# Optimization experiments

Measured on AMD Instinct MI355X. Metric: run time of the kernel, lower is better.

## Reference

```python
import jax, jax.numpy as jnp
import numpy as np

B, NAV, H, W = 16, 36, 120, 160
HID, AEMB, NF = 512, 32, 4

def _conv(x, w, b, stride, pad, dil, groups):
    y = jax.lax.conv_general_dilated(x, w, stride, pad, rhs_dilation=dil, feature_group_count=groups)
    return y + b[None, :, None, None]

def _avgpool(x, k, s):
    y = jax.lax.reduce_window(x, 0.0, jax.lax.add, (1, 1) + k, (1, 1) + s, 'VALID')
    return y / float(k[0] * k[1])

def _conv2_block(x, w1, b1, w2, b2):
    # conv2_1: k5 stride (5,7) dilation 10 -> avgpool 3/3 -> conv2_2: k3 stride 2 dilation (1,2) -> avgpool (3,9)/3
    y = _conv(x, w1, b1, (5, 7), ((0, 0), (0, 0)), (10, 10), 1)
    y = _avgpool(y, (3, 3), (3, 3))
    y = _conv(y, w2, b2, (2, 2), ((0, 0), (0, 0)), (1, 2), 1)
    y = _avgpool(y, (3, 9), (3, 3))
    return y[:, 0]  # [B,3,12]

def setup_inputs() -> dict:
    key = jax.random.key(0)
    ks = jax.random.split(key, 24)
    s = 0.02
    d = {}
    d['depth_feat_0'] = jax.random.normal(ks[0], (B, NAV, H, W), jnp.float32)
    d['depth_feat_1'] = jax.random.normal(ks[1], (B, NAV, H, W), jnp.float32)
    d['obj_detection_feat'] = jax.random.normal(ks[2], (B, NAV, H, W), jnp.float32)
    d['num_navigable_feat'] = jax.random.uniform(ks[3], (B, NAV), jnp.float32)
    d['pre_action_feat'] = jax.random.normal(ks[4], (B, AEMB), jnp.float32)
    d['h_0'] = jax.random.normal(ks[5], (B, HID), jnp.float32)
    d['c_0'] = jax.random.normal(ks[6], (B, HID), jnp.float32)
    d['weighted_ctx'] = jax.random.normal(ks[7], (B, HID), jnp.float32)
    d['navigable_index'] = jax.random.randint(ks[8], (B, 8), 0, NAV).astype(jnp.int32)
    # params
    d['conv1_w'] = jax.random.normal(ks[9], (NAV, 2, 5, 5), jnp.float32) * s
    d['conv1_b'] = jnp.zeros((NAV,), jnp.float32)
    d['dyn_filters'] = jax.random.normal(ks[10], (NF, NAV, 2, 5, 5), jnp.float32) * s
    d['dyn_w1'] = jax.random.normal(ks[11], (HID, HID // 4), jnp.float32) * s
    d['dyn_b1'] = jnp.zeros((HID // 4,), jnp.float32)
    d['dyn_w2'] = jax.random.normal(ks[12], (HID // 4, NF), jnp.float32) * s
    d['dyn_b2'] = jnp.zeros((NF,), jnp.float32)
    d['conv2_1_w'] = jax.random.normal(ks[13], (1, 1, 5, 5), jnp.float32) * s
    d['conv2_1_b'] = jnp.zeros((1,), jnp.float32)
    d['conv2_2_w'] = jax.random.normal(ks[14], (1, 1, 3, 3), jnp.float32) * s
    d['conv2_2_b'] = jnp.zeros((1,), jnp.float32)
    in_sz = HID + NAV + NF + AEMB  # 584
    d['lstm_w_ih'] = jax.random.normal(ks[15], (4 * HID, in_sz), jnp.float32) * s
    d['lstm_w_hh'] = jax.random.normal(ks[16], (4 * HID, HID), jnp.float32) * s
    d['lstm_b_ih'] = jnp.zeros((4 * HID,), jnp.float32)
    d['lstm_b_hh'] = jnp.zeros((4 * HID,), jnp.float32)
    return d

def reference(depth_feat_0, depth_feat_1, obj_detection_feat, num_navigable_feat, pre_action_feat, h_0, c_0, weighted_ctx, navigable_index, conv1_w, conv1_b, dyn_filters, dyn_w1, dyn_b1, dyn_w2, dyn_b2, conv2_1_w, conv2_1_b, conv2_2_w, conv2_2_b, lstm_w_ih, lstm_w_hh, lstm_b_ih, lstm_b_hh):
    Bv = depth_feat_0.shape[0]
    # interleave depth channels: [B,72,H,W] (replaces 36-iter python copy loop)
    mid1 = jnp.stack([depth_feat_0, depth_feat_1], axis=2).reshape(Bv, 2 * NAV, H, W)
    total_depth = _conv(mid1, conv1_w, conv1_b, (1, 1), ((2, 2), (2, 2)), (1, 1), NAV)  # [B,36,H,W]
    nav_attn = jax.nn.softmax(num_navigable_feat, axis=1)[:, :, None, None]
    mid2 = jnp.stack([total_depth * nav_attn, obj_detection_feat * nav_attn], axis=2).reshape(Bv, 2 * NAV, H, W)
    # dynamic conv: per-sample filter = attention-weighted mix of NF learned grouped filters
    filt_attn = jax.nn.softmax(jax.nn.relu(weighted_ctx @ dyn_w1 + dyn_b1) @ dyn_w2 + dyn_b2, axis=1)  # [B,4]
    kern = jnp.einsum('bf,fgikl->bgikl', filt_attn, dyn_filters).reshape(Bv * NAV, 2, 5, 5)
    dyn_out = jax.lax.conv_general_dilated(mid2.reshape(1, Bv * 2 * NAV, H, W), kern, (1, 1), ((2, 2), (2, 2)), feature_group_count=Bv * NAV).reshape(Bv, NAV, H, W)
    # panorama canvas assembly: tile i -> row block (2 - i//12), col i%12
    canvas = dyn_out.reshape(Bv, 3, 12, H, W)[:, ::-1].transpose(0, 1, 3, 2, 4).reshape(Bv, 1, 3 * H, 12 * W)
    v1 = _conv2_block(canvas, conv2_1_w, conv2_1_b, conv2_2_w, conv2_2_b)
    rolled = jnp.concatenate([canvas[..., -W:], canvas[..., :-W]], axis=-1)
    v2 = _conv2_block(rolled, conv2_1_w, conv2_1_b, conv2_2_w, conv2_2_b)
    v2 = jnp.concatenate([v2[:, :, 1:], v2[:, :, :1]], axis=-1)
    vf = ((v1 + v2) * 0.5)[:, ::-1].reshape(Bv, NAV)  # flip row dim then flatten
    vf = jax.nn.softmax(vf / 10.0, axis=1)  # self.softmax_temperature hardcoded to 10
    concat = jnp.concatenate([weighted_ctx, vf, filt_attn, pre_action_feat], axis=1)
    gates = concat @ lstm_w_ih.T + lstm_b_ih + h_0 @ lstm_w_hh.T + lstm_b_hh
    i, f, g, o = jnp.split(gates, 4, axis=1)
    c_1 = jax.nn.sigmoid(f) * c_0 + jax.nn.sigmoid(i) * jnp.tanh(g)
    h_1 = jax.nn.sigmoid(o) * jnp.tanh(c_1)
    mask = jnp.zeros((Bv, NAV + 1), jnp.float32).at[:, 0].set(1.0)
    mask = mask.at[jnp.arange(Bv)[:, None], navigable_index + 1].set(1.0)
    return (h_1, c_1, vf, mask)
```

## Files before the change

### kernel.cpp

```cpp
#include <hip/hip_runtime.h>
#include <math.h>

#define B_ 16
#define NAV_ 36
#define H_ 120
#define W_ 160
#define HID_ 512
#define PLANES (B_*NAV_)
#define PLANE_PX (H_*W_)
#define CANVAS_H 360
#define CANVAS_W 1920
#define CANVAS_PX (CANVAS_H*CANVAS_W)

#define OUT_H 12
#define IN_ROWS 20
#define TD_ROWS 16
#define OBJ_ROWS 16
#define ROWB 352
#define INCH (IN_ROWS*ROWB)

#define WS_NAV    0
#define WS_FATT   576
#define WS_KERN   640
#define WS_TD     29440
#define WS_CANVAS (WS_TD + PLANES*PLANE_PX)
#define WS_POOL1  (WS_CANVAS + B_*CANVAS_PX)
#define WS_VF     (WS_POOL1 + B_*2*19*89)

typedef unsigned int u32;
typedef _Float16 h2_t __attribute__((ext_vector_type(2)));
typedef float float4a __attribute__((ext_vector_type(4), aligned(4)));

__device__ __forceinline__ float sigmoidf_(float x) { return 1.f / (1.f + expf(-x)); }

__device__ __forceinline__ u32 pkh(float a, float b) {
    return __builtin_bit_cast(u32, __builtin_amdgcn_cvt_pkrtz(a, b));
}
__device__ __forceinline__ float dot2h(u32 a, u32 b, float c) {
#if __has_builtin(__builtin_amdgcn_fdot2)
    return __builtin_amdgcn_fdot2(__builtin_bit_cast(h2_t, a),
                                  __builtin_bit_cast(h2_t, b), c, false);
#else
    float r;
    asm("v_dot2_f32_f16 %0, %1, %2, %3" : "=v"(r) : "v"(a), "v"(b), "v"(c));
    return r;
#endif
}

__device__ __forceinline__ void conv8(const unsigned char* b0, const unsigned char* b1,
                                      const u32* ew, float* acc)
{
    #pragma unroll
    for (int ky = 0; ky < 5; ++ky) {
        const int off = ky*ROWB;
        int4 qa = *(const int4*)(b0 + off);
        int2 qb = *(const int2*)(b0 + off + 16);
        int4 ra = *(const int4*)(b1 + off);
        int2 rb = *(const int2*)(b1 + off + 16);
        u32 P[6] = {(u32)qa.x,(u32)qa.y,(u32)qa.z,(u32)qa.w,(u32)qb.x,(u32)qb.y};
        u32 Q[6] = {(u32)ra.x,(u32)ra.y,(u32)ra.z,(u32)ra.w,(u32)rb.x,(u32)rb.y};
        const u32 e0 = ew[ky*3+0], e1 = ew[ky*3+1], e2 = ew[ky*3+2];
        const u32 f0 = ew[15+ky*3+0], f1 = ew[15+ky*3+1], f2 = ew[15+ky*3+2];
        const u32 o0 = e0 << 16;
        const u32 o1 = __builtin_amdgcn_alignbit(e1, e0, 16);
        const u32 o2 = __builtin_amdgcn_alignbit(e2, e1, 16);
        const u32 g0 = f0 << 16;
        const u32 g1 = __builtin_amdgcn_alignbit(f1, f0, 16);
        const u32 g2 = __builtin_amdgcn_alignbit(f2, f1, 16);
        #pragma unroll
        for (int m = 0; m < 4; ++m) {
            acc[2*m]   = dot2h(e0, P[m], dot2h(e1, P[m+1], dot2h(e2, P[m+2], acc[2*m])));
            acc[2*m+1] = dot2h(o0, P[m], dot2h(o1, P[m+1], dot2h(o2, P[m+2], acc[2*m+1])));
            acc[2*m]   = dot2h(f0, Q[m], dot2h(f1, Q[m+1], dot2h(f2, Q[m+2], acc[2*m])));
            acc[2*m+1] = dot2h(g0, Q[m], dot2h(g1, Q[m+1], dot2h(g2, Q[m+2], acc[2*m+1])));
        }
    }
}

#define LOAD_EW(EW, SW)                                                        \
    {                                                                          \
        _Pragma("unroll")                                                      \
        for (int q = 0; q < 7; ++q) {                                          \
            int4 t_ = ((const int4*)(SW))[q];                                  \
            EW[4*q]=(u32)t_.x; EW[4*q+1]=(u32)t_.y; EW[4*q+2]=(u32)t_.z; EW[4*q+3]=(u32)t_.w; \
        }                                                                      \
        int2 t_ = ((const int2*)(SW))[14];                                     \
        EW[28]=(u32)t_.x; EW[29]=(u32)t_.y;                                    \
    }

__global__ __launch_bounds__(256)
void k_pre(const float* __restrict__ wctx, const float* __restrict__ dw1,
           const float* __restrict__ db1, const float* __restrict__ dw2,
           const float* __restrict__ db2, const float* __restrict__ dynf,
           const float* __restrict__ numnav, float* __restrict__ ws)
{
    const int tid = threadIdx.x;
    const int b = blockIdx.x;
    __shared__ float sh[128];
    __shared__ float sred[8];
    __shared__ float nv[36];
    __shared__ float nms[2];
    if (tid < 128) {
        float acc = db1[tid];
        for (int k = 0; k < HID_; ++k) acc += wctx[b*HID_ + k] * dw1[k*128 + tid];
        sh[tid] = fmaxf(acc, 0.f);
    }
    __syncthreads();
    if (tid < 4) {
        float acc = db2[tid];
        for (int j = 0; j < 128; ++j) acc += sh[j] * dw2[j*4 + tid];
        sred[tid] = acc;
    }
    __syncthreads();
    if (tid == 0) {
        float m = fmaxf(fmaxf(sred[0], sred[1]), fmaxf(sred[2], sred[3]));
        float e0 = expf(sred[0]-m), e1 = expf(sred[1]-m), e2 = expf(sred[2]-m), e3 = expf(sred[3]-m);
        float s = e0+e1+e2+e3;
        sred[4] = e0/s; sred[5] = e1/s; sred[6] = e2/s; sred[7] = e3/s;
        ws[WS_FATT + b*4+0] = sred[4]; ws[WS_FATT + b*4+1] = sred[5];
        ws[WS_FATT + b*4+2] = sred[6]; ws[WS_FATT + b*4+3] = sred[7];
    }
    __syncthreads();
    {
        const float fa0 = sred[4], fa1 = sred[5], fa2 = sred[6], fa3 = sred[7];
        for (int e = tid; e < 1800; e += 256) {
            float v = fa0*dynf[e] + fa1*dynf[1800+e] + fa2*dynf[3600+e] + fa3*dynf[5400+e];
            ws[WS_KERN + b*1800 + e] = v;
        }
    }
    if (tid < 36) nv[tid] = numnav[b*NAV_ + tid];
    __syncthreads();
    if (tid == 0) {
        float m = nv[0];
        for (int i = 1; i < 36; ++i) m = fmaxf(m, nv[i]);
        float s = 0.f;
        for (int i = 0; i < 36; ++i) s += expf(nv[i]-m);
        nms[0] = m; nms[1] = s;
    }
    __syncthreads();
    if (tid < 36) ws[WS_NAV + b*NAV_ + tid] = expf(nv[tid]-nms[0]) / nms[1];
}

__global__ __launch_bounds__(256)
void k_fused(const float* __restrict__ d0, const float* __restrict__ d1,
             const float* __restrict__ obj, const float* __restrict__ conv1_w,
             const float* __restrict__ conv1_b, float* __restrict__ ws)
{
    const int tid = threadIdx.x;
    const int band = blockIdx.x;
    const int plane = blockIdx.y;
    const int b = plane / NAV_;
    const int g = plane % NAV_;
    const int r0 = band * OUT_H;

    __shared__ __align__(16) unsigned char smem[2*INCH + OBJ_ROWS*ROWB + TD_ROWS*ROWB + 256];
    unsigned char* inL  = smem;
    unsigned char* objL = smem + 2*INCH;
    unsigned char* tdL  = objL + OBJ_ROWS*ROWB;
    u32* wts = (u32*)(tdL + TD_ROWS*ROWB);

    if (tid < 30) {
        const int ch = tid/15, ky = (tid%15)/3, k = tid%3;
        const float* wsrc = conv1_w + g*50 + ch*25 + ky*5;
        wts[tid] = pkh(wsrc[2*k], (k < 2) ? wsrc[2*k+1] : 0.f);
    } else if (tid >= 32 && tid < 62) {
        const int t2 = tid - 32;
        const int ch = t2/15, ky = (t2%15)/3, k = t2%3;
        const float* wsrc = ws + WS_KERN + plane*50 + ch*25 + ky*5;
        wts[tid] = pkh(wsrc[2*k], (k < 2) ? wsrc[2*k+1] : 0.f);
    } else if (tid == 62) ((float*)wts)[62] = conv1_b[g];
    else if (tid == 63)   ((float*)wts)[63] = ws[WS_NAV + plane];

    const float* pd0 = d0 + (size_t)plane*PLANE_PX;
    const float* pd1 = d1 + (size_t)plane*PLANE_PX;
    const float* pob = obj + (size_t)plane*PLANE_PX;
    for (int i = tid; i < 2*IN_ROWS*44 + OBJ_ROWS*44; i += 256) {
        const float* src; unsigned char* dst; int row, j, gr;
        if (i < 2*IN_ROWS*44) {
            const int ch = i/(IN_ROWS*44), rem = i%(IN_ROWS*44);
            row = rem/44; j = rem%44; gr = r0 - 4 + row;
            src = ch ? pd1 : pd0;
            dst = inL + (size_t)ch*INCH + row*ROWB + j*8;
        } else {
            const int k = i - 2*IN_ROWS*44;
            row = k/44; j = k%44; gr = r0 - 2 + row;
            src = pob;
            dst = objL + row*ROWB + j*8;
        }
        u32 lo = 0, hi = 0;
        if ((unsigned)gr < (unsigned)H_ && j <= 40) {
            const float* sp = src + gr*W_;
            if (j == 0) hi = pkh(sp[0], sp[1]);
            else if (j < 40) { const float4a v = *(const float4a*)(sp + 4*j - 2);
                               lo = pkh(v.x, v.y);  hi = pkh(v.z, v.w); }
            else lo = pkh(sp[158], sp[159]);
        }
        *(int2*)dst = make_int2((int)lo, (int)hi);
    }
    if (tid < 32) {
        const int rr = tid >> 1;
        *(u32*)(tdL + rr*ROWB + ((tid & 1) ? 324 : 0)) = 0;
    }
    __syncthreads();

    for (int t = tid; t < TD_ROWS*20; t += 256) {
        const int tr = t/20, s = t%20;
        const int gr = r0 - 2 + tr;
        u32* rowp = (u32*)(tdL + tr*ROWB);
        if ((unsigned)gr >= (unsigned)H_) {
            rowp[4*s+1] = 0;
            *(int2*)(rowp + 4*s + 2) = make_int2(0, 0);
            rowp[4*s+4] = 0;
            continue;
        }
        float acc[8];
        #pragma unroll
        for (int p = 0; p < 8; ++p) acc[p] = 0.f;
        u32 ew[30];
        LOAD_EW(ew, wts)
        conv8(inL + tr*ROWB + s*16, inL + INCH + tr*ROWB + s*16, ew, acc);
        const float bias = ((const float*)wts)[62];
        const u32 p0 = pkh(acc[0]+bias, acc[1]+bias);
        const u32 p1 = pkh(acc[2]+bias, acc[3]+bias);
        const u32 p2 = pkh(acc[4]+bias, acc[5]+bias);
        const u32 p3 = pkh(acc[6]+bias, acc[7]+bias);
        rowp[4*s+1] = p0;
        *(int2*)(rowp + 4*s + 2) = make_int2((int)p1, (int)p2);
        rowp[4*s+4] = p3;
    }
    __syncthreads();

    if (tid < OUT_H*20) {
        const int yr = tid/20, s = tid%20;
        float acc[8];
        #pragma unroll
        for (int p = 0; p < 8; ++p) acc[p] = 0.f;
        u32 ew[30];
        LOAD_EW(ew, wts + 32)
        conv8(tdL + yr*ROWB + s*16, objL + yr*ROWB + s*16, ew, acc);
        const float a = ((const float*)wts)[63];
        const int rowblk = 2 - g/12;
        const int colblk = g % 12;
        float* cbase = ws + WS_CANVAS + (size_t)b*CANVAS_PX
                     + (size_t)(rowblk*H_ + r0 + yr)*CANVAS_W + colblk*W_ + s*8;
        *(float4*)cbase     = make_float4(a*acc[0], a*acc[1], a*acc[2], a*acc[3]);
        *(float4*)(cbase+4) = make_float4(a*acc[4], a*acc[5], a*acc[6], a*acc[7]);
    }
}

__global__ __launch_bounds__(256)
void k_conv2a(const float* __restrict__ w21p, const float* __restrict__ b21p,
              float* __restrict__ ws)
{
    const int blk = blockIdx.x;
    const int a = blk % 19;
    const int bv = blk / 19;
    const int ver = bv & 1;
    const int b = bv >> 1;
    const int coloff = ver ? (CANVAS_W - W_) : 0;

    __shared__ float s1[3*267];
    __shared__ float swt[25];
    if (threadIdx.x < 25) swt[threadIdx.x] = w21p[threadIdx.x];
    __syncthreads();
    const float b21 = b21p[0];
    const float* cv = ws + WS_CANVAS + (size_t)b*CANVAS_PX;

    for (int px = threadIdx.x; px < 3*267; px += 256) {
        const int row = px / 267;
        const int v = px % 267;
        const int u = 3*a + row;
        float acc = b21;
        #pragma unroll
        for (int ky = 0; ky < 5; ++ky) {
            const float* rp = cv + (5*u + 10*ky)*CANVAS_W;
            #pragma unroll
            for (int kx = 0; kx < 5; ++kx) {
                int c = 7*v + 10*kx + coloff;
                if (c >= CANVAS_W) c -= CANVAS_W;
                acc += swt[ky*5+kx] * rp[c];
            }
        }
        s1[px] = acc;
    }
    __syncthreads();
    if (threadIdx.x < 89) {
        const int bb = threadIdx.x;
        float s = 0.f;
        #pragma unroll
        for (int i = 0; i < 3; ++i)
            #pragma unroll
            for (int j = 0; j < 3; ++j)
                s += s1[i*267 + 3*bb + j];
        ws[WS_POOL1 + blk*89 + bb] = s * (1.f/9.f);
    }
}

__global__ __launch_bounds__(256)
void k_conv2b(const float* __restrict__ w22p, const float* __restrict__ b22p,
              const int* __restrict__ navidx, float* __restrict__ ws,
              float* __restrict__ out)
{
    const int b = blockIdx.x;
    __shared__ float p[2*19*89];
    __shared__ float s2[2*9*43];
    __shared__ float svf[36];
    __shared__ float sms[2];
    __shared__ float swt[9];

    for (int i = threadIdx.x; i < 2*19*89; i += 256)
        p[i] = ws[WS_POOL1 + (b*2)*19*89 + i];
    if (threadIdx.x < 9) swt[threadIdx.x] = w22p[threadIdx.x];
    const float b22 = b22p[0];
    __syncthreads();

    for (int t = threadIdx.x; t < 2*9*43; t += 256) {
        const int ver = t / 387;
        const int r = t % 387;
        const int pp = r / 43;
        const int q = r % 43;
        float acc = b22;
        #pragma unroll
        for (int i = 0; i < 3; ++i)
            #pragma unroll
            for (int j = 0; j < 3; ++j)
                acc += swt[i*3+j] * p[(ver*19 + (2*pp+i))*89 + 2*q + 2*j];
        s2[ver*387 + pp*43 + q] = acc;
    }
    __syncthreads();

    if (threadIdx.x < 36) {
        const int gg = threadIdx.x;
        const int io = 2 - gg/12;
        const int j  = gg % 12;
        const int j2 = (j + 1) % 12;
        float s = 0.f;
        #pragma unroll
        for (int ii = 0; ii < 3; ++ii)
            #pragma unroll
            for (int jj = 0; jj < 9; ++jj)
                s += s2[(3*io+ii)*43 + 3*j + jj] + s2[387 + (3*io+ii)*43 + 3*j2 + jj];
        svf[gg] = s * (0.5f/27.f);
    }
    __syncthreads();
    if (threadIdx.x == 0) {
        float m = svf[0];
        for (int i = 1; i < 36; ++i) m = fmaxf(m, svf[i]);
        float s = 0.f;
        for (int i = 0; i < 36; ++i) s += expf((svf[i]-m)*0.1f);
        sms[0] = m; sms[1] = s;
    }
    __syncthreads();
    if (threadIdx.x < 36) {
        const float v = expf((svf[threadIdx.x]-sms[0])*0.1f) / sms[1];
        ws[WS_VF + b*36 + threadIdx.x] = v;
        out[16384 + b*36 + threadIdx.x] = v;
    }
    if (threadIdx.x < 37) {
        const int j = threadIdx.x;
        float v = (j == 0) ? 1.f : 0.f;
        #pragma unroll
        for (int t = 0; t < 8; ++t)
            if (navidx[b*8+t] + 1 == j) v = 1.f;
        out[16960 + b*37 + j] = v;
    }
}

#define CT_STRIDE 20
__global__ __launch_bounds__(256)
void k_lstm(const float* __restrict__ wctx, const float* __restrict__ pre_action,
            const float* __restrict__ h0, const float* __restrict__ c0,
            const float* __restrict__ w_ih, const float* __restrict__ w_hh,
            const float* __restrict__ b_ih, const float* __restrict__ b_hh,
            const float* __restrict__ ws, float* __restrict__ out)
{
    __shared__ float cT[1096*CT_STRIDE];
    __shared__ float red[8*32*16];
    __shared__ float gatev[8][16];
    const int tid = threadIdx.x;

    for (int idx = tid; idx < 1096*16; idx += 256) {
        const int k = idx >> 4;
        const int bb = idx & 15;
        float v;
        if (k < 512)       v = wctx[bb*512 + k];
        else if (k < 548)  v = ws[WS_VF + bb*36 + (k-512)];
        else if (k < 552)  v = ws[WS_FATT + bb*4 + (k-548)];
        else if (k < 584)  v = pre_action[bb*32 + (k-552)];
        else               v = h0[bb*512 + (k-584)];
        cT[k*CT_STRIDE + bb] = v;
    }
    __syncthreads();

    const int rl = tid >> 5;
    const int lane = tid & 31;
    const int u0 = blockIdx.x*2;
    const int ul = rl & 1;
    const int gate = rl >> 1;
    const int r = u0 + ul + gate*512;

    float acc[16];
    #pragma unroll
    for (int i = 0; i < 16; ++i) acc[i] = 0.f;

    const float* wih_r = w_ih + (size_t)r*584;
    for (int k = lane; k < 584; k += 32) {
        const float wv = wih_r[k];
        const float* cp = cT + k*CT_STRIDE;
        #pragma unroll
        for (int i = 0; i < 16; ++i) acc[i] += wv*cp[i];
    }
    const float* whh_r = w_hh + (size_t)r*512;
    for (int k = lane; k < 512; k += 32) {
        const float wv = whh_r[k];
        const float* cp = cT + (584+k)*CT_STRIDE;
        #pragma unroll
        for (int i = 0; i < 16; ++i) acc[i] += wv*cp[i];
    }
    float* rp = red + (rl*32 + lane)*16;
    #pragma unroll
    for (int i = 0; i < 16; ++i) rp[i] = acc[i];
    __syncthreads();

    if (tid < 128) {
        const int rr = tid >> 4;
        const int bb = tid & 15;
        const int rrow = u0 + (rr & 1) + (rr >> 1)*512;
        float s = b_ih[rrow] + b_hh[rrow];
        for (int l = 0; l < 32; ++l) s += red[(rr*32 + l)*16 + bb];
        gatev[rr][bb] = s;
    }
    __syncthreads();

    if (tid < 32) {
        const int ul2 = tid >> 4;
        const int bb = tid & 15;
        const int u = u0 + ul2;
        const float gi = gatev[0+ul2][bb];
        const float gf = gatev[2+ul2][bb];
        const float gg = gatev[4+ul2][bb];
        const float go = gatev[6+ul2][bb];
        const float c1 = sigmoidf_(gf)*c0[bb*512+u] + sigmoidf_(gi)*tanhf(gg);
        const float h1 = sigmoidf_(go)*tanhf(c1);
        out[bb*512 + u] = h1;
        out[8192 + bb*512 + u] = c1;
    }
}

extern "C" void kernel_launch(void* const* d_in, const int* in_sizes, int n_in,
                              void* d_out, int out_size, void* d_ws, size_t ws_size,
                              hipStream_t stream)
{
    const float* d0        = (const float*)d_in[0];
    const float* d1        = (const float*)d_in[1];
    const float* obj       = (const float*)d_in[2];
    const float* numnav    = (const float*)d_in[3];
    const float* preact    = (const float*)d_in[4];
    const float* h0        = (const float*)d_in[5];
    const float* c0        = (const float*)d_in[6];
    const float* wctx      = (const float*)d_in[7];
    const int*   navidx    = (const int*)d_in[8];
    const float* conv1_w   = (const float*)d_in[9];
    const float* conv1_b   = (const float*)d_in[10];
    const float* dynf      = (const float*)d_in[11];
    const float* dw1       = (const float*)d_in[12];
    const float* db1       = (const float*)d_in[13];
    const float* dw2       = (const float*)d_in[14];
    const float* db2       = (const float*)d_in[15];
    const float* w21       = (const float*)d_in[16];
    const float* b21       = (const float*)d_in[17];
    const float* w22       = (const float*)d_in[18];
    const float* b22       = (const float*)d_in[19];
    const float* wih       = (const float*)d_in[20];
    const float* whh       = (const float*)d_in[21];
    const float* bih       = (const float*)d_in[22];
    const float* bhh       = (const float*)d_in[23];
    float* ws  = (float*)d_ws;
    float* out = (float*)d_out;

    dim3 blk(256);
    k_pre   <<<dim3(16),      blk, 0, stream>>>(wctx, dw1, db1, dw2, db2, dynf, numnav, ws);
    k_fused <<<dim3(10, 576), blk, 0, stream>>>(d0, d1, obj, conv1_w, conv1_b, ws);
    k_conv2a<<<dim3(608),     blk, 0, stream>>>(w21, b21, ws);
    k_conv2b<<<dim3(16),      blk, 0, stream>>>(w22, b22, navidx, ws, out);
    k_lstm  <<<dim3(256),     blk, 0, stream>>>(wctx, preact, h0, c0, wih, whh,
                                                bih, bhh, ws, out);
}
```

Measured before the change: 159.6 us.

## Process five row bands per block with register-prefetched next-band loads

```diff
diff --git a/kernel.cpp b/kernel.cpp
--- a/kernel.cpp
+++ b/kernel.cpp
@@ -18,6 +18,8 @@
 #define OBJ_ROWS 16
 #define ROWB 352
 #define INCH (IN_ROWS*ROWB)
+#define NSLOT (2*IN_ROWS*44 + OBJ_ROWS*44)
+#define SPT 10
 
 #define WS_NAV    0
 #define WS_FATT   576
@@ -147,11 +149,11 @@
              const float* __restrict__ conv1_b, float* __restrict__ ws)
 {
     const int tid = threadIdx.x;
-    const int band = blockIdx.x;
+    const int half = blockIdx.x;
     const int plane = blockIdx.y;
     const int b = plane / NAV_;
     const int g = plane % NAV_;
-    const int r0 = band * OUT_H;
+    const int r0base = half * 5 * OUT_H;
 
     __shared__ __align__(16) unsigned char smem[2*INCH + OBJ_ROWS*ROWB + TD_ROWS*ROWB + 256];
     unsigned char* inL  = smem;
@@ -170,81 +172,130 @@
         wts[tid] = pkh(wsrc[2*k], (k < 2) ? wsrc[2*k+1] : 0.f);
     } else if (tid == 62) ((float*)wts)[62] = conv1_b[g];
     else if (tid == 63)   ((float*)wts)[63] = ws[WS_NAV + plane];
+    if (tid >= 64 && tid < 96) {
+        const int t2 = tid - 64;
+        const int rr = t2 >> 1;
+        *(u32*)(tdL + rr*ROWB + ((t2 & 1) ? 324 : 0)) = 0;
+    }
 
     const float* pd0 = d0 + (size_t)plane*PLANE_PX;
     const float* pd1 = d1 + (size_t)plane*PLANE_PX;
     const float* pob = obj + (size_t)plane*PLANE_PX;
-    for (int i = tid; i < 2*IN_ROWS*44 + OBJ_ROWS*44; i += 256) {
-        const float* src; unsigned char* dst; int row, j, gr;
-        if (i < 2*IN_ROWS*44) {
-            const int ch = i/(IN_ROWS*44), rem = i%(IN_ROWS*44);
-            row = rem/44; j = rem%44; gr = r0 - 4 + row;
-            src = ch ? pd1 : pd0;
-            dst = inL + (size_t)ch*INCH + row*ROWB + j*8;
-        } else {
-            const int k = i - 2*IN_ROWS*44;
-            row = k/44; j = k%44; gr = r0 - 2 + row;
-            src = pob;
-            dst = objL + row*ROWB + j*8;
-        }
-        u32 lo = 0, hi = 0;
-        if ((unsigned)gr < (unsigned)H_ && j <= 40) {
-            const float* sp = src + gr*W_;
-            if (j == 0) hi = pkh(sp[0], sp[1]);
-            else if (j < 40) { const float4a v = *(const float4a*)(sp + 4*j - 2);
-                               lo = pkh(v.x, v.y);  hi = pkh(v.z, v.w); }
-            else lo = pkh(sp[158], sp[159]);
-        }
-        *(int2*)dst = make_int2((int)lo, (int)hi);
-    }
-    if (tid < 32) {
-        const int rr = tid >> 1;
-        *(u32*)(tdL + rr*ROWB + ((tid & 1) ? 324 : 0)) = 0;
-    }
-    __syncthreads();
-
-    for (int t = tid; t < TD_ROWS*20; t += 256) {
-        const int tr = t/20, s = t%20;
-        const int gr = r0 - 2 + tr;
-        u32* rowp = (u32*)(tdL + tr*ROWB);
-        if ((unsigned)gr >= (unsigned)H_) {
-            rowp[4*s+1] = 0;
-            *(int2*)(rowp + 4*s + 2) = make_int2(0, 0);
-            rowp[4*s+4] = 0;
-            continue;
-        }
-        float acc[8];
-        #pragma unroll
-        for (int p = 0; p < 8; ++p) acc[p] = 0.f;
-        u32 ew[30];
-        LOAD_EW(ew, wts)
-        conv8(inL + tr*ROWB + s*16, inL + INCH + tr*ROWB + s*16, ew, acc);
-        const float bias = ((const float*)wts)[62];
-        const u32 p0 = pkh(acc[0]+bias, acc[1]+bias);
-        const u32 p1 = pkh(acc[2]+bias, acc[3]+bias);
-        const u32 p2 = pkh(acc[4]+bias, acc[5]+bias);
-        const u32 p3 = pkh(acc[6]+bias, acc[7]+bias);
-        rowp[4*s+1] = p0;
-        *(int2*)(rowp + 4*s + 2) = make_int2((int)p1, (int)p2);
-        rowp[4*s+4] = p3;
-    }
-    __syncthreads();
-
-    if (tid < OUT_H*20) {
-        const int yr = tid/20, s = tid%20;
-        float acc[8];
-        #pragma unroll
-        for (int p = 0; p < 8; ++p) acc[p] = 0.f;
-        u32 ew[30];
-        LOAD_EW(ew, wts + 32)
-        conv8(tdL + yr*ROWB + s*16, objL + yr*ROWB + s*16, ew, acc);
-        const float a = ((const float*)wts)[63];
-        const int rowblk = 2 - g/12;
-        const int colblk = g % 12;
-        float* cbase = ws + WS_CANVAS + (size_t)b*CANVAS_PX
-                     + (size_t)(rowblk*H_ + r0 + yr)*CANVAS_W + colblk*W_ + s*8;
-        *(float4*)cbase     = make_float4(a*acc[0], a*acc[1], a*acc[2], a*acc[3]);
-        *(float4*)(cbase+4) = make_float4(a*acc[4], a*acc[5], a*acc[6], a*acc[7]);
+
+    u32 meta[SPT];
+    #pragma unroll
+    for (int k = 0; k < SPT; ++k) {
+        const int slot = tid + 256*k;
+        u32 m = 0;
+        if (slot < NSLOT) {
+            int j, rr4, ss; u32 dst;
+            if (slot < 2*IN_ROWS*44) {
+                const int ch = slot / (IN_ROWS*44);
+                const int rem = slot % (IN_ROWS*44);
+                const int row = rem / 44;
+                j = rem % 44; rr4 = row; ss = ch;
+                dst = (u32)(ch*INCH + row*ROWB + j*8);
+            } else {
+                const int s2 = slot - 2*IN_ROWS*44;
+                const int row = s2 / 44;
+                j = s2 % 44; rr4 = row + 2; ss = 2;
+                dst = (u32)(2*INCH + row*ROWB + j*8);
+            }
+            m = dst | ((u32)j << 15) | ((u32)rr4 << 21) | ((u32)ss << 26) | 0x80000000u;
+        }
+        meta[k] = m;
+    }
+
+    float4a pf[SPT];
+    const float4a z4 = {0.f, 0.f, 0.f, 0.f};
+
+    #define ISSUE(R0) {                                                        \
+        _Pragma("unroll")                                                      \
+        for (int k = 0; k < SPT; ++k) {                                        \
+            float4a v = z4;                                                    \
+            if (meta[k] & 0x80000000u) {                                       \
+                const int j   = (int)((meta[k] >> 15) & 63u);                  \
+                const int gr  = (R0) + (int)((meta[k] >> 21) & 31u) - 4;       \
+                const int ss  = (int)((meta[k] >> 26) & 3u);                   \
+                if ((unsigned)gr < (unsigned)H_ && j <= 40) {                  \
+                    const float* src = (ss == 0) ? pd0 : ((ss == 1) ? pd1 : pob); \
+                    const int co = (j == 0) ? 0 : ((j < 40) ? 4*j - 2 : 156);  \
+                    v = *(const float4a*)(src + gr*W_ + co);                   \
+                }                                                              \
+            }                                                                  \
+            pf[k] = v;                                                         \
+        } }
+
+    #define WRITEPF() {                                                        \
+        _Pragma("unroll")                                                      \
+        for (int k = 0; k < SPT; ++k) {                                        \
+            if (meta[k] & 0x80000000u) {                                       \
+                const int j = (int)((meta[k] >> 15) & 63u);                    \
+                u32 lo = 0, hi = 0;                                            \
+                if (j == 0)       { hi = pkh(pf[k].x, pf[k].y); }              \
+                else if (j < 40)  { lo = pkh(pf[k].x, pf[k].y); hi = pkh(pf[k].z, pf[k].w); } \
+                else if (j == 40) { lo = pkh(pf[k].z, pf[k].w); }              \
+                *(int2*)(smem + (meta[k] & 0x7FFFu)) = make_int2((int)lo, (int)hi); \
+            }                                                                  \
+        } }
+
+    ISSUE(r0base)
+    WRITEPF()
+    __syncthreads();
+
+    for (int band = 0; band < 5; ++band) {
+        const int r0 = r0base + band*OUT_H;
+        if (band < 4) ISSUE(r0 + OUT_H)
+
+        for (int t = tid; t < TD_ROWS*20; t += 256) {
+            const int tr = t/20, s = t%20;
+            const int gr = r0 - 2 + tr;
+            u32* rowp = (u32*)(tdL + tr*ROWB);
+            if ((unsigned)gr >= (unsigned)H_) {
+                rowp[4*s+1] = 0;
+                *(int2*)(rowp + 4*s + 2) = make_int2(0, 0);
+                rowp[4*s+4] = 0;
+                continue;
+            }
+            float acc[8];
+            #pragma unroll
+            for (int p = 0; p < 8; ++p) acc[p] = 0.f;
+            u32 ew[30];
+            LOAD_EW(ew, wts)
+            conv8(inL + tr*ROWB + s*16, inL + INCH + tr*ROWB + s*16, ew, acc);
+            const float bias = ((const float*)wts)[62];
+            const u32 p0 = pkh(acc[0]+bias, acc[1]+bias);
+            const u32 p1 = pkh(acc[2]+bias, acc[3]+bias);
+            const u32 p2 = pkh(acc[4]+bias, acc[5]+bias);
+            const u32 p3 = pkh(acc[6]+bias, acc[7]+bias);
+            rowp[4*s+1] = p0;
+            *(int2*)(rowp + 4*s + 2) = make_int2((int)p1, (int)p2);
+            rowp[4*s+4] = p3;
+        }
+        __syncthreads();
+
+        if (tid < OUT_H*20) {
+            const int yr = tid/20, s = tid%20;
+            float acc[8];
+            #pragma unroll
+            for (int p = 0; p < 8; ++p) acc[p] = 0.f;
+            u32 ew[30];
+            LOAD_EW(ew, wts + 32)
+            conv8(tdL + yr*ROWB + s*16, objL + yr*ROWB + s*16, ew, acc);
+            const float a = ((const float*)wts)[63];
+            const int rowblk = 2 - g/12;
+            const int colblk = g % 12;
+            float* cbase = ws + WS_CANVAS + (size_t)b*CANVAS_PX
+                         + (size_t)(rowblk*H_ + r0 + yr)*CANVAS_W + colblk*W_ + s*8;
+            *(float4*)cbase     = make_float4(a*acc[0], a*acc[1], a*acc[2], a*acc[3]);
+            *(float4*)(cbase+4) = make_float4(a*acc[4], a*acc[5], a*acc[6], a*acc[7]);
+        }
+        __syncthreads();
+
+        if (band < 4) {
+            WRITEPF()
+            __syncthreads();
+        }
     }
 }
 
@@ -480,7 +531,7 @@
 
     dim3 blk(256);
     k_pre   <<<dim3(16),      blk, 0, stream>>>(wctx, dw1, db1, dw2, db2, dynf, numnav, ws);
-    k_fused <<<dim3(10, 576), blk, 0, stream>>>(d0, d1, obj, conv1_w, conv1_b, ws);
+    k_fused <<<dim3(2, 576),  blk, 0, stream>>>(d0, d1, obj, conv1_w, conv1_b, ws);
     k_conv2a<<<dim3(608),     blk, 0, stream>>>(w21, b21, ws);
     k_conv2b<<<dim3(16),      blk, 0, stream>>>(w22, b22, navidx, ws, out);
     k_lstm  <<<dim3(256),     blk, 0, stream>>>(wctx, preact, h0, c0, wih, whh,
```

Result: faster. 146.6 us (-8.2%).
